# Kernel tuning notes

Hardware: AMD Instinct MI355X
Metric: run time of the kernel (lower is better)

Reference implementation:

```python
import jax, jax.numpy as jnp
import numpy as np

B, S, H, I, E = 4, 4096, 1024, 4096, 4
VOCAB = 32000


def setup_inputs() -> dict:
    key = jax.random.key(0)
    k1, k2, k3, k4, k5 = jax.random.split(key, 5)
    scale = 1.0 / np.sqrt(H)
    return {
        "hidden_states": jax.random.normal(k1, (B, S, H), dtype=jnp.float32),
        "gate_proj": jax.random.normal(k2, (E, H, I), dtype=jnp.float32) * scale,
        "up_proj": jax.random.normal(k3, (E, H, I), dtype=jnp.float32) * scale,
        "down_proj": jax.random.normal(k4, (E, I, H), dtype=jnp.float32) * (1.0 / np.sqrt(I)),
        "token_ids": jax.random.randint(k5, (B, S), 0, VOCAB, dtype=jnp.int64),
    }


def reference(hidden_states, gate_proj, up_proj, down_proj, token_ids):
    # hidden_states: [B, S, H]; token_ids: [B, S]
    num_experts = gate_proj.shape[0]
    expert_ids = token_ids % num_experts  # [B, S]
    out = jnp.zeros_like(hidden_states)
    for e in range(num_experts):  # small fixed expert loop
        gate = jax.nn.silu(jnp.einsum("bsh,hi->bsi", hidden_states, gate_proj[e]))
        up = jnp.einsum("bsh,hi->bsi", hidden_states, up_proj[e])
        y = jnp.einsum("bsi,ih->bsh", gate * up, down_proj[e])
        out = jnp.where((expert_ids == e)[..., None], y, out)
    return out
```

## Files before the change

### kernel.cpp

```cpp
#include <hip/hip_runtime.h>

#define TOK    16384
#define HD     1024
#define ID     4096
#define NE     4
#define MAXMT  131
#define MAXMT2 67
#define NKT    (HD / 64)

typedef __attribute__((ext_vector_type(4))) float f32x4;
typedef __attribute__((ext_vector_type(8))) short bf16x8;
typedef unsigned int u32;

static __device__ __forceinline__ unsigned short f2bf(float f) {
  unsigned u = __float_as_uint(f);
  u += 0x7FFFu + ((u >> 16) & 1u);
  return (unsigned short)(u >> 16);
}

static __device__ __forceinline__ void gl16(const void* g, void* l) {
  __builtin_amdgcn_global_load_lds((const __attribute__((address_space(1))) u32*)g,
                                   (__attribute__((address_space(3))) u32*)l, 16, 0, 0);
}

static __device__ __forceinline__ void barx() {
  asm volatile("" ::: "memory");
  __builtin_amdgcn_s_barrier();
  asm volatile("" ::: "memory");
}

__global__ void k_route0(const int* __restrict__ ids, int* __restrict__ meta) {
  __shared__ int cnt[4];
  int t = threadIdx.x;
  if (t < 4) cnt[t] = 0;
  __syncthreads();
  int l0 = 0, l1 = 0, l2 = 0, l3 = 0;
  for (int i = t; i < TOK; i += 256) {
    int e = ids[i] & 3;
    l0 += (e == 0); l1 += (e == 1); l2 += (e == 2); l3 += (e == 3);
  }
  atomicAdd(&cnt[0], l0); atomicAdd(&cnt[1], l1);
  atomicAdd(&cnt[2], l2); atomicAdd(&cnt[3], l3);
  __syncthreads();
  if (t == 0) {
    int o = 0;
    for (int e = 0; e < 4; ++e) { meta[e] = o; meta[8 + e] = o; o += cnt[e]; }
    meta[4] = o;
  }
}

__global__ void k_route1(const int* __restrict__ ids, int* __restrict__ meta,
                         int* __restrict__ perm) {
  int i = blockIdx.x * 256 + threadIdx.x;
  if (i < TOK) {
    int e = ids[i] & 3;
    int s = atomicAdd(&meta[8 + e], 1);
    perm[s] = i;
  }
}

__global__ void k_pre(const float* __restrict__ gw, const float* __restrict__ uw,
                      const float* __restrict__ dw, const float* __restrict__ hs,
                      unsigned short* __restrict__ gT, unsigned short* __restrict__ uT,
                      unsigned short* __restrict__ dT, unsigned short* __restrict__ hid) {
  int z = blockIdx.y;
  int t = threadIdx.x;
  if (z >= 12) {
    int i = ((z - 12) * 1024 + blockIdx.x) * 256 + t;
    const f32x4* p = (const f32x4*)(hs + ((size_t)i << 3));
    f32x4 a = p[0], b = p[1];
    union { unsigned short u[8]; uint4 q; } o;
    o.u[0] = f2bf(a.x); o.u[1] = f2bf(a.y); o.u[2] = f2bf(a.z); o.u[3] = f2bf(a.w);
    o.u[4] = f2bf(b.x); o.u[5] = f2bf(b.y); o.u[6] = f2bf(b.z); o.u[7] = f2bf(b.w);
    *(uint4*)(hid + ((size_t)i << 3)) = o.q;
    return;
  }
  __shared__ float tile[64][65];
  const float* s; unsigned short* d; int R, C, lg;
  if (z < 8) {
    R = HD; C = ID; lg = 6;
    int m = z & 3;
    if (z < 4) { s = gw + (size_t)m * R * C; d = gT + (size_t)m * R * C; }
    else       { s = uw + (size_t)m * R * C; d = uT + (size_t)m * R * C; }
  } else {
    R = ID; C = HD; lg = 4;
    int m = z - 8;
    s = dw + (size_t)m * R * C; d = dT + (size_t)m * R * C;
  }
  int bx = blockIdx.x;
  int tx = bx & ((1 << lg) - 1), ty = bx >> lg;
  int r0 = ty << 6, c0 = tx << 6;
  int lr = t >> 4, lc = (t & 15) << 2;
  #pragma unroll
  for (int it = 0; it < 4; ++it) {
    int r = lr + (it << 4);
    f32x4 v = *(const f32x4*)(s + (size_t)(r0 + r) * C + c0 + lc);
    tile[r][lc] = v.x; tile[r][lc + 1] = v.y; tile[r][lc + 2] = v.z; tile[r][lc + 3] = v.w;
  }
  __syncthreads();
  int c = t >> 2, rb = (t & 3) << 4;
  union { unsigned short u[16]; uint4 q[2]; } o;
  #pragma unroll
  for (int j = 0; j < 16; ++j) o.u[j] = f2bf(tile[rb + j][c]);
  uint4* dp = (uint4*)(d + (size_t)(c0 + c) * R + r0 + rb);
  dp[0] = o.q[0]; dp[1] = o.q[1];
}

#define MFMA16 __builtin_amdgcn_mfma_f32_16x16x32_bf16

#define RD_A(MH, KX, D) { _Pragma("unroll") for (int m = 0; m < 4; ++m) \
  fa[m] = *(const bf16x8*)(smem + (D) + ((offA[m] + (MH) * 8192) ^ ((KX) << 6))); }
#define RD_B(KX, D) { _Pragma("unroll") for (int n = 0; n < 4; ++n) \
  fb[n] = *(const bf16x8*)(smem + (D) + (offB[n] ^ ((KX) << 6))); }
#define STG_A(HH, TILE, D) { _Pragma("unroll") for (int j = (HH) * 2; j < (HH) * 2 + 2; ++j) \
  gl16(srcA[j] + (TILE) * 64, smem + (D) + dstA[j]); }
#define STG_B(HH, TILE, D) { _Pragma("unroll") for (int j = (HH) * 2; j < (HH) * 2 + 2; ++j) \
  gl16(srcB[j] + (TILE) * 64, smem + (D) + dstB[j]); }
#define PH_TAIL(MH) barx(); \
  asm volatile("s_waitcnt lgkmcnt(0)" ::: "memory"); \
  __builtin_amdgcn_sched_barrier(0); \
  __builtin_amdgcn_s_setprio(1); \
  { _Pragma("unroll") for (int m = 0; m < 4; ++m) \
    _Pragma("unroll") for (int n = 0; n < 4; ++n) \
      acc[(MH) * 4 + m][n] = MFMA16(fa[m], fb[n], acc[(MH) * 4 + m][n], 0, 0, 0); } \
  __builtin_amdgcn_s_setprio(0)

__global__ __launch_bounds__(512, 2) void k_gemm1(
    const unsigned short* __restrict__ hid,
    const unsigned short* __restrict__ gT,
    const unsigned short* __restrict__ uT,
    const int* __restrict__ meta,
    const int* __restrict__ perm,
    unsigned short* __restrict__ act) {
  extern __shared__ __align__(16) char smem[];
  int offs[5];
  #pragma unroll
  for (int i = 0; i < 5; ++i) offs[i] = meta[i];
  int bid = blockIdx.x;
  int logical = (bid & 7) * (MAXMT2 * 32 / 8) + (bid >> 3);
  int mt = logical >> 5;
  int ny = logical & 31;
  int e = -1, mloc = 0, base = 0;
  #pragma unroll
  for (int ee = 0; ee < 4; ++ee) {
    int tiles = (offs[ee + 1] - offs[ee] + 255) >> 8;
    if (e < 0 && mt < base + tiles) { e = ee; mloc = mt - base; }
    base += tiles;
  }
  if (e < 0) return;
  int slot0 = offs[e] + (mloc << 8);
  int send = offs[e + 1];
  int tid = threadIdx.x, lane = tid & 63, wid = tid >> 6;
  int n0 = ny << 7;

  int rsub = lane >> 3;
  int ke = ((lane & 7) ^ rsub) << 3;
  const unsigned short* srcA[4];
  const unsigned short* srcB[4];
  int dstA[4], dstB[4];
  const unsigned short* gb = gT + (size_t)e * ID * HD;
  const unsigned short* ub = uT + (size_t)e * ID * HD;
  #pragma unroll
  for (int j = 0; j < 4; ++j) {
    int r = j * 64 + wid * 8 + rsub;
    int slot = slot0 + r;
    int pr = perm[slot < send ? slot : slot0];
    srcA[j] = hid + (size_t)pr * HD + ke;
    dstA[j] = j * 8192 + wid * 1024;
    int rb = r;
    int s = rb >> 4;
    int grow = n0 + ((s >> 1) << 4) + (rb & 15);
    srcB[j] = ((s & 1) ? ub : gb) + (size_t)grow * HD + ke;
    dstB[j] = 32768 + j * 8192 + wid * 1024;
  }

  int wm = wid >> 2, wn = wid & 3;
  int r16 = lane & 15, kg = lane >> 4;
  int offA[4], offB[4];
  #pragma unroll
  for (int m = 0; m < 4; ++m) {
    int row = wm * 128 + m * 16 + r16;
    offA[m] = row * 128 + ((kg << 4) ^ ((row & 7) << 4));
  }
  #pragma unroll
  for (int n = 0; n < 4; ++n) {
    int row = wn * 64 + n * 16 + r16;
    offB[n] = 32768 + row * 128 + ((kg << 4) ^ ((row & 7) << 4));
  }

  f32x4 acc[8][4];
  #pragma unroll
  for (int m = 0; m < 8; ++m)
    #pragma unroll
    for (int n = 0; n < 4; ++n) acc[m][n] = (f32x4){0.f, 0.f, 0.f, 0.f};
  bf16x8 fa[4], fb[4];

  STG_B(0, 0, 0);
  STG_A(0, 0, 0); STG_A(1, 0, 0);
  STG_B(1, 0, 0);
  STG_B(0, 1, 65536);
  asm volatile("s_waitcnt vmcnt(2)" ::: "memory");
  barx();

  #pragma unroll 1
  for (int i = 0; i < NKT / 2 - 1; ++i) {
    int t1 = 2 * i + 1, t2 = 2 * i + 2, t3 = 2 * i + 3;
    RD_A(0, 0, 0); RD_B(0, 0);
    STG_B(1, t1, 65536);
    PH_TAIL(0); barx();
    RD_A(1, 0, 0);
    STG_A(0, t1, 65536); STG_A(1, t1, 65536);
    PH_TAIL(1); barx();
    RD_A(0, 1, 0); RD_B(1, 0);
    PH_TAIL(0); barx();
    RD_A(1, 1, 0);
    STG_B(0, t2, 0);
    PH_TAIL(1);
    asm volatile("s_waitcnt vmcnt(2)" ::: "memory");
    barx();
    RD_A(0, 0, 65536); RD_B(0, 65536);
    STG_A(0, t2, 0); STG_A(1, t2, 0);
    PH_TAIL(0); barx();
    RD_A(1, 0, 65536);
    STG_B(1, t2, 0);
    PH_TAIL(1); barx();
    RD_A(0, 1, 65536); RD_B(1, 65536);
    PH_TAIL(0); barx();
    RD_A(1, 1, 65536);
    STG_B(0, t3, 65536);
    PH_TAIL(1);
    asm volatile("s_waitcnt vmcnt(2)" ::: "memory");
    barx();
  }
  {
    RD_A(0, 0, 0); RD_B(0, 0);
    STG_B(1, 15, 65536);
    PH_TAIL(0); barx();
    RD_A(1, 0, 0);
    STG_A(0, 15, 65536); STG_A(1, 15, 65536);
    PH_TAIL(1); barx();
    RD_A(0, 1, 0); RD_B(1, 0);
    PH_TAIL(0); barx();
    RD_A(1, 1, 0);
    PH_TAIL(1);
    asm volatile("s_waitcnt vmcnt(0)" ::: "memory");
    barx();
    RD_A(0, 0, 65536); RD_B(0, 65536);
    PH_TAIL(0); barx();
    RD_A(1, 0, 65536);
    PH_TAIL(1); barx();
    RD_A(0, 1, 65536); RD_B(1, 65536);
    PH_TAIL(0); barx();
    RD_A(1, 1, 65536);
    PH_TAIL(1);
  }

  #pragma unroll
  for (int mf = 0; mf < 8; ++mf) {
    int lr = wm * 128 + mf * 16 + kg * 4;
    #pragma unroll
    for (int np = 0; np < 2; ++np) {
      int col = n0 + (2 * wn + np) * 16 + r16;
      #pragma unroll
      for (int r = 0; r < 4; ++r) {
        int slot = slot0 + lr + r;
        if (slot < send) {
          float g = acc[mf][2 * np][r];
          float u = acc[mf][2 * np + 1][r];
          float y = (g / (1.f + __expf(-g))) * u;
          act[(size_t)slot * ID + col] = f2bf(y);
        }
      }
    }
  }
}

__global__ __launch_bounds__(256, 2) void k_gemm2(
    const unsigned short* __restrict__ act,
    const unsigned short* __restrict__ dT,
    const int* __restrict__ meta,
    const int* __restrict__ perm,
    float* __restrict__ out) {
  __shared__ unsigned short As[128 * 64];
  __shared__ unsigned short Bs[128 * 64];
  int offs[5];
  #pragma unroll
  for (int i = 0; i < 5; ++i) offs[i] = meta[i];
  int bid = blockIdx.x;
  int logical = (bid & 7) * (MAXMT * 8 / 8) + (bid >> 3);
  int mt = logical >> 3;
  int nyy = logical & 7;
  int e = -1, mloc = 0, base = 0;
  #pragma unroll
  for (int ee = 0; ee < 4; ++ee) {
    int tiles = (offs[ee + 1] - offs[ee] + 127) >> 7;
    if (e < 0 && mt < base + tiles) { e = ee; mloc = mt - base; }
    base += tiles;
  }
  if (e < 0) return;
  int slot0 = offs[e] + (mloc << 7);
  int send = offs[e + 1];
  int tid = threadIdx.x;
  int n0 = nyy << 7;
  const unsigned short* dbase = dT + (size_t)e * HD * ID;
  const unsigned short* ap[4];
  const unsigned short* bp[4];
  int wofs[4];
  #pragma unroll
  for (int it = 0; it < 4; ++it) {
    int b = (tid << 4) + (it << 12);
    int row = b >> 7;
    int kob = b & 127;
    int slot = slot0 + row;
    int s2 = slot < send ? slot : slot0;
    ap[it] = act + (size_t)s2 * ID + (kob >> 1);
    bp[it] = dbase + (size_t)(n0 + row) * ID + (kob >> 1);
    wofs[it] = row * 64 + ((kob ^ ((row & 7) << 4)) >> 1);
  }
  int lane = tid & 63, wid = tid >> 6;
  int wm = wid >> 1, wn = wid & 1;
  int r16 = lane & 15, kg = lane >> 4;
  f32x4 zero = {0.f, 0.f, 0.f, 0.f};
  f32x4 acc[4][4];
  #pragma unroll
  for (int m = 0; m < 4; ++m)
    #pragma unroll
    for (int n = 0; n < 4; ++n) acc[m][n] = zero;

  bf16x8 sa[4], sb[4];
  #pragma unroll
  for (int it = 0; it < 4; ++it) {
    sa[it] = *(const bf16x8*)(ap[it]);
    sb[it] = *(const bf16x8*)(bp[it]);
  }
  for (int kt = 0; kt < ID / 64; ++kt) {
    __syncthreads();
    #pragma unroll
    for (int it = 0; it < 4; ++it) {
      *(bf16x8*)(As + wofs[it]) = sa[it];
      *(bf16x8*)(Bs + wofs[it]) = sb[it];
    }
    __syncthreads();
    if (kt < ID / 64 - 1) {
      int ko = (kt + 1) << 6;
      #pragma unroll
      for (int it = 0; it < 4; ++it) {
        sa[it] = *(const bf16x8*)(ap[it] + ko);
        sb[it] = *(const bf16x8*)(bp[it] + ko);
      }
    }
    #pragma unroll
    for (int kk = 0; kk < 2; ++kk) {
      bf16x8 fa[4], fb[4];
      #pragma unroll
      for (int m = 0; m < 4; ++m) {
        int row = (wm << 6) + (m << 4) + r16;
        int kob = (kk << 6) + (kg << 4);
        fa[m] = *(const bf16x8*)(As + row * 64 + ((kob ^ ((row & 7) << 4)) >> 1));
      }
      #pragma unroll
      for (int n = 0; n < 4; ++n) {
        int row = (wn << 6) + (n << 4) + r16;
        int kob = (kk << 6) + (kg << 4);
        fb[n] = *(const bf16x8*)(Bs + row * 64 + ((kob ^ ((row & 7) << 4)) >> 1));
      }
      #pragma unroll
      for (int m = 0; m < 4; ++m)
        #pragma unroll
        for (int n = 0; n < 4; ++n)
          acc[m][n] = __builtin_amdgcn_mfma_f32_16x16x32_bf16(fa[m], fb[n], acc[m][n], 0, 0, 0);
    }
  }
  #pragma unroll
  for (int m = 0; m < 4; ++m) {
    int lr = (wm << 6) + (m << 4) + (kg << 2);
    int pr4[4];
    #pragma unroll
    for (int r = 0; r < 4; ++r) {
      int slot = slot0 + lr + r;
      pr4[r] = slot < send ? perm[slot] : -1;
    }
    #pragma unroll
    for (int n = 0; n < 4; ++n) {
      int col = n0 + (wn << 6) + (n << 4) + r16;
      #pragma unroll
      for (int r = 0; r < 4; ++r) {
        if (pr4[r] >= 0) out[(size_t)pr4[r] * HD + col] = acc[m][n][r];
      }
    }
  }
}

extern "C" void kernel_launch(void* const* d_in, const int* in_sizes, int n_in,
                              void* d_out, int out_size, void* d_ws, size_t ws_size,
                              hipStream_t stream) {
  const float* hs = (const float*)d_in[0];
  const float* gw = (const float*)d_in[1];
  const float* uw = (const float*)d_in[2];
  const float* dw = (const float*)d_in[3];
  const int* ids = (const int*)d_in[4];
  float* out = (float*)d_out;

  char* w = (char*)d_ws;
  size_t o = 0;
  int* meta = (int*)(w + o); o += 64;
  int* perm = (int*)(w + o); o += (size_t)TOK * 4;
  o = (o + 255) & ~(size_t)255;
  unsigned short* hid = (unsigned short*)(w + o); o += (size_t)TOK * HD * 2;
  unsigned short* gT  = (unsigned short*)(w + o); o += (size_t)NE * ID * HD * 2;
  unsigned short* uT  = (unsigned short*)(w + o); o += (size_t)NE * ID * HD * 2;
  unsigned short* dT  = (unsigned short*)(w + o); o += (size_t)NE * ID * HD * 2;
  unsigned short* actb = (unsigned short*)(w + o); o += (size_t)TOK * ID * 2;

  hipFuncSetAttribute((const void*)k_gemm1,
                      hipFuncAttributeMaxDynamicSharedMemorySize, 131072);

  hipLaunchKernelGGL(k_route0, dim3(1), dim3(256), 0, stream, ids, meta);
  hipLaunchKernelGGL(k_route1, dim3(TOK / 256), dim3(256), 0, stream, ids, meta, perm);
  hipLaunchKernelGGL(k_pre, dim3(1024, 20), dim3(256), 0, stream,
                     gw, uw, dw, hs, gT, uT, dT, hid);
  hipLaunchKernelGGL(k_gemm1, dim3(MAXMT2 * 32), dim3(512), 131072, stream,
                     hid, gT, uT, meta, perm, actb);
  hipLaunchKernelGGL(k_gemm2, dim3(MAXMT * 8), dim3(256), 0, stream,
                     actb, dT, meta, perm, out);
}
```

Baseline: 644.3 us.

## Convert both expert GEMMs to persistent kernels with atomic tile queues

Both GEMM kernels now launch a fixed grid (256 and 512 workgroups) and loop, pulling tile indices from a global atomic counter that the routing kernel resets each call. The goal is to cut the cost of launching many empty or padded workgroups and to balance load across CUs dynamically. The old XCD-aware bid swizzle is gone, so tiles are handed out in linear order. That may hurt L2 locality on the multi-XCD chip, and each tile now pays for an extra atomic and two barriers.

Result: slower. 692.3 us (+7.4%).

```diff
diff --git a/kernel.cpp b/kernel.cpp
--- a/kernel.cpp
+++ b/kernel.cpp
@@ -7,6 +7,8 @@
 #define MAXMT  131
 #define MAXMT2 67
 #define NKT    (HD / 64)
+#define NT1    (MAXMT2 * 32)
+#define NT2    (MAXMT * 8)
 
 typedef __attribute__((ext_vector_type(4))) float f32x4;
 typedef __attribute__((ext_vector_type(8))) short bf16x8;
@@ -29,7 +31,8 @@
   asm volatile("" ::: "memory");
 }
 
-__global__ void k_route0(const int* __restrict__ ids, int* __restrict__ meta) {
+__global__ void k_route0(const int* __restrict__ ids, int* __restrict__ meta,
+                         int* __restrict__ ctrs) {
   __shared__ int cnt[4];
   int t = threadIdx.x;
   if (t < 4) cnt[t] = 0;
@@ -46,6 +49,8 @@
     int o = 0;
     for (int e = 0; e < 4; ++e) { meta[e] = o; meta[8 + e] = o; o += cnt[e]; }
     meta[4] = o;
+    ctrs[0] = 0;
+    ctrs[1] = 0;
   }
 }
 
@@ -131,49 +136,23 @@
     const unsigned short* __restrict__ uT,
     const int* __restrict__ meta,
     const int* __restrict__ perm,
-    unsigned short* __restrict__ act) {
+    unsigned short* __restrict__ act,
+    int* ctr) {
   extern __shared__ __align__(16) char smem[];
+  __shared__ int s_t;
   int offs[5];
   #pragma unroll
   for (int i = 0; i < 5; ++i) offs[i] = meta[i];
-  int bid = blockIdx.x;
-  int logical = (bid & 7) * (MAXMT2 * 32 / 8) + (bid >> 3);
-  int mt = logical >> 5;
-  int ny = logical & 31;
-  int e = -1, mloc = 0, base = 0;
-  #pragma unroll
-  for (int ee = 0; ee < 4; ++ee) {
-    int tiles = (offs[ee + 1] - offs[ee] + 255) >> 8;
-    if (e < 0 && mt < base + tiles) { e = ee; mloc = mt - base; }
-    base += tiles;
-  }
-  if (e < 0) return;
-  int slot0 = offs[e] + (mloc << 8);
-  int send = offs[e + 1];
   int tid = threadIdx.x, lane = tid & 63, wid = tid >> 6;
-  int n0 = ny << 7;
 
   int rsub = lane >> 3;
   int ke = ((lane & 7) ^ rsub) << 3;
-  const unsigned short* srcA[4];
-  const unsigned short* srcB[4];
   int dstA[4], dstB[4];
-  const unsigned short* gb = gT + (size_t)e * ID * HD;
-  const unsigned short* ub = uT + (size_t)e * ID * HD;
   #pragma unroll
   for (int j = 0; j < 4; ++j) {
-    int r = j * 64 + wid * 8 + rsub;
-    int slot = slot0 + r;
-    int pr = perm[slot < send ? slot : slot0];
-    srcA[j] = hid + (size_t)pr * HD + ke;
     dstA[j] = j * 8192 + wid * 1024;
-    int rb = r;
-    int s = rb >> 4;
-    int grow = n0 + ((s >> 1) << 4) + (rb & 15);
-    srcB[j] = ((s & 1) ? ub : gb) + (size_t)grow * HD + ke;
     dstB[j] = 32768 + j * 8192 + wid * 1024;
   }
-
   int wm = wid >> 2, wn = wid & 3;
   int r16 = lane & 15, kg = lane >> 4;
   int offA[4], offB[4];
@@ -187,88 +166,124 @@
     int row = wn * 64 + n * 16 + r16;
     offB[n] = 32768 + row * 128 + ((kg << 4) ^ ((row & 7) << 4));
   }
-
-  f32x4 acc[8][4];
-  #pragma unroll
-  for (int m = 0; m < 8; ++m)
-    #pragma unroll
-    for (int n = 0; n < 4; ++n) acc[m][n] = (f32x4){0.f, 0.f, 0.f, 0.f};
   bf16x8 fa[4], fb[4];
 
-  STG_B(0, 0, 0);
-  STG_A(0, 0, 0); STG_A(1, 0, 0);
-  STG_B(1, 0, 0);
-  STG_B(0, 1, 65536);
-  asm volatile("s_waitcnt vmcnt(2)" ::: "memory");
-  barx();
-
-  #pragma unroll 1
-  for (int i = 0; i < NKT / 2 - 1; ++i) {
-    int t1 = 2 * i + 1, t2 = 2 * i + 2, t3 = 2 * i + 3;
-    RD_A(0, 0, 0); RD_B(0, 0);
-    STG_B(1, t1, 65536);
-    PH_TAIL(0); barx();
-    RD_A(1, 0, 0);
-    STG_A(0, t1, 65536); STG_A(1, t1, 65536);
-    PH_TAIL(1); barx();
-    RD_A(0, 1, 0); RD_B(1, 0);
-    PH_TAIL(0); barx();
-    RD_A(1, 1, 0);
-    STG_B(0, t2, 0);
-    PH_TAIL(1);
+  for (;;) {
+    __syncthreads();
+    if (tid == 0) s_t = atomicAdd(ctr, 1);
+    __syncthreads();
+    int tt = s_t;
+    if (tt >= NT1) break;
+    int mt = tt >> 5;
+    int ny = tt & 31;
+    int e = -1, mloc = 0, base = 0;
+    #pragma unroll
+    for (int ee = 0; ee < 4; ++ee) {
+      int tiles = (offs[ee + 1] - offs[ee] + 255) >> 8;
+      if (e < 0 && mt < base + tiles) { e = ee; mloc = mt - base; }
+      base += tiles;
+    }
+    if (e < 0) continue;
+    int slot0 = offs[e] + (mloc << 8);
+    int send = offs[e + 1];
+    int n0 = ny << 7;
+
+    const unsigned short* srcA[4];
+    const unsigned short* srcB[4];
+    const unsigned short* gb = gT + (size_t)e * ID * HD;
+    const unsigned short* ub = uT + (size_t)e * ID * HD;
+    #pragma unroll
+    for (int j = 0; j < 4; ++j) {
+      int r = j * 64 + wid * 8 + rsub;
+      int slot = slot0 + r;
+      int pr = perm[slot < send ? slot : slot0];
+      srcA[j] = hid + (size_t)pr * HD + ke;
+      int s = r >> 4;
+      int grow = n0 + ((s >> 1) << 4) + (r & 15);
+      srcB[j] = ((s & 1) ? ub : gb) + (size_t)grow * HD + ke;
+    }
+
+    f32x4 acc[8][4];
+    #pragma unroll
+    for (int m = 0; m < 8; ++m)
+      #pragma unroll
+      for (int n = 0; n < 4; ++n) acc[m][n] = (f32x4){0.f, 0.f, 0.f, 0.f};
+
+    STG_B(0, 0, 0);
+    STG_A(0, 0, 0); STG_A(1, 0, 0);
+    STG_B(1, 0, 0);
+    STG_B(0, 1, 65536);
     asm volatile("s_waitcnt vmcnt(2)" ::: "memory");
     barx();
-    RD_A(0, 0, 65536); RD_B(0, 65536);
-    STG_A(0, t2, 0); STG_A(1, t2, 0);
-    PH_TAIL(0); barx();
-    RD_A(1, 0, 65536);
-    STG_B(1, t2, 0);
-    PH_TAIL(1); barx();
-    RD_A(0, 1, 65536); RD_B(1, 65536);
-    PH_TAIL(0); barx();
-    RD_A(1, 1, 65536);
-    STG_B(0, t3, 65536);
-    PH_TAIL(1);
-    asm volatile("s_waitcnt vmcnt(2)" ::: "memory");
-    barx();
-  }
-  {
-    RD_A(0, 0, 0); RD_B(0, 0);
-    STG_B(1, 15, 65536);
-    PH_TAIL(0); barx();
-    RD_A(1, 0, 0);
-    STG_A(0, 15, 65536); STG_A(1, 15, 65536);
-    PH_TAIL(1); barx();
-    RD_A(0, 1, 0); RD_B(1, 0);
-    PH_TAIL(0); barx();
-    RD_A(1, 1, 0);
-    PH_TAIL(1);
-    asm volatile("s_waitcnt vmcnt(0)" ::: "memory");
-    barx();
-    RD_A(0, 0, 65536); RD_B(0, 65536);
-    PH_TAIL(0); barx();
-    RD_A(1, 0, 65536);
-    PH_TAIL(1); barx();
-    RD_A(0, 1, 65536); RD_B(1, 65536);
-    PH_TAIL(0); barx();
-    RD_A(1, 1, 65536);
-    PH_TAIL(1);
-  }
-
-  #pragma unroll
-  for (int mf = 0; mf < 8; ++mf) {
-    int lr = wm * 128 + mf * 16 + kg * 4;
-    #pragma unroll
-    for (int np = 0; np < 2; ++np) {
-      int col = n0 + (2 * wn + np) * 16 + r16;
-      #pragma unroll
-      for (int r = 0; r < 4; ++r) {
-        int slot = slot0 + lr + r;
-        if (slot < send) {
-          float g = acc[mf][2 * np][r];
-          float u = acc[mf][2 * np + 1][r];
-          float y = (g / (1.f + __expf(-g))) * u;
-          act[(size_t)slot * ID + col] = f2bf(y);
+
+    #pragma unroll 1
+    for (int i = 0; i < NKT / 2 - 1; ++i) {
+      int t1 = 2 * i + 1, t2 = 2 * i + 2, t3 = 2 * i + 3;
+      RD_A(0, 0, 0); RD_B(0, 0);
+      STG_B(1, t1, 65536);
+      PH_TAIL(0); barx();
+      RD_A(1, 0, 0);
+      STG_A(0, t1, 65536); STG_A(1, t1, 65536);
+      PH_TAIL(1); barx();
+      RD_A(0, 1, 0); RD_B(1, 0);
+      PH_TAIL(0); barx();
+      RD_A(1, 1, 0);
+      STG_B(0, t2, 0);
+      PH_TAIL(1);
+      asm volatile("s_waitcnt vmcnt(2)" ::: "memory");
+      barx();
+      RD_A(0, 0, 65536); RD_B(0, 65536);
+      STG_A(0, t2, 0); STG_A(1, t2, 0);
+      PH_TAIL(0); barx();
+      RD_A(1, 0, 65536);
+      STG_B(1, t2, 0);
+      PH_TAIL(1); barx();
+      RD_A(0, 1, 65536); RD_B(1, 65536);
+      PH_TAIL(0); barx();
+      RD_A(1, 1, 65536);
+      STG_B(0, t3, 65536);
+      PH_TAIL(1);
+      asm volatile("s_waitcnt vmcnt(2)" ::: "memory");
+      barx();
+    }
+    {
+      RD_A(0, 0, 0); RD_B(0, 0);
+      STG_B(1, 15, 65536);
+      PH_TAIL(0); barx();
+      RD_A(1, 0, 0);
+      STG_A(0, 15, 65536); STG_A(1, 15, 65536);
+      PH_TAIL(1); barx();
+      RD_A(0, 1, 0); RD_B(1, 0);
+      PH_TAIL(0); barx();
+      RD_A(1, 1, 0);
+      PH_TAIL(1);
+      asm volatile("s_waitcnt vmcnt(0)" ::: "memory");
+      barx();
+      RD_A(0, 0, 65536); RD_B(0, 65536);
+      PH_TAIL(0); barx();
+      RD_A(1, 0, 65536);
+      PH_TAIL(1); barx();
+      RD_A(0, 1, 65536); RD_B(1, 65536);
+      PH_TAIL(0); barx();
+      RD_A(1, 1, 65536);
+      PH_TAIL(1);
+    }
+
+    #pragma unroll
+    for (int mf = 0; mf < 8; ++mf) {
+      int lr = wm * 128 + mf * 16 + kg * 4;
+      #pragma unroll
+      for (int np = 0; np < 2; ++np) {
+        int col = n0 + (2 * wn + np) * 16 + r16;
+        #pragma unroll
+        for (int r = 0; r < 4; ++r) {
+          int slot = slot0 + lr + r;
+          if (slot < send) {
+            float g = acc[mf][2 * np][r];
+            float u = acc[mf][2 * np + 1][r];
+            float y = (g / (1.f + __expf(-g))) * u;
+            act[(size_t)slot * ID + col] = f2bf(y);
+          }
         }
       }
     }
@@ -280,112 +295,125 @@
     const unsigned short* __restrict__ dT,
     const int* __restrict__ meta,
     const int* __restrict__ perm,
-    float* __restrict__ out) {
+    float* __restrict__ out,
+    int* ctr) {
   __shared__ unsigned short As[128 * 64];
   __shared__ unsigned short Bs[128 * 64];
+  __shared__ int s_t;
   int offs[5];
   #pragma unroll
   for (int i = 0; i < 5; ++i) offs[i] = meta[i];
-  int bid = blockIdx.x;
-  int logical = (bid & 7) * (MAXMT * 8 / 8) + (bid >> 3);
-  int mt = logical >> 3;
-  int nyy = logical & 7;
-  int e = -1, mloc = 0, base = 0;
-  #pragma unroll
-  for (int ee = 0; ee < 4; ++ee) {
-    int tiles = (offs[ee + 1] - offs[ee] + 127) >> 7;
-    if (e < 0 && mt < base + tiles) { e = ee; mloc = mt - base; }
-    base += tiles;
-  }
-  if (e < 0) return;
-  int slot0 = offs[e] + (mloc << 7);
-  int send = offs[e + 1];
   int tid = threadIdx.x;
-  int n0 = nyy << 7;
-  const unsigned short* dbase = dT + (size_t)e * HD * ID;
-  const unsigned short* ap[4];
-  const unsigned short* bp[4];
+  int lane = tid & 63, wid = tid >> 6;
+  int wm = wid >> 1, wn = wid & 1;
+  int r16 = lane & 15, kg = lane >> 4;
   int wofs[4];
   #pragma unroll
   for (int it = 0; it < 4; ++it) {
     int b = (tid << 4) + (it << 12);
     int row = b >> 7;
     int kob = b & 127;
-    int slot = slot0 + row;
-    int s2 = slot < send ? slot : slot0;
-    ap[it] = act + (size_t)s2 * ID + (kob >> 1);
-    bp[it] = dbase + (size_t)(n0 + row) * ID + (kob >> 1);
     wofs[it] = row * 64 + ((kob ^ ((row & 7) << 4)) >> 1);
   }
-  int lane = tid & 63, wid = tid >> 6;
-  int wm = wid >> 1, wn = wid & 1;
-  int r16 = lane & 15, kg = lane >> 4;
-  f32x4 zero = {0.f, 0.f, 0.f, 0.f};
-  f32x4 acc[4][4];
-  #pragma unroll
-  for (int m = 0; m < 4; ++m)
-    #pragma unroll
-    for (int n = 0; n < 4; ++n) acc[m][n] = zero;
-
-  bf16x8 sa[4], sb[4];
-  #pragma unroll
-  for (int it = 0; it < 4; ++it) {
-    sa[it] = *(const bf16x8*)(ap[it]);
-    sb[it] = *(const bf16x8*)(bp[it]);
-  }
-  for (int kt = 0; kt < ID / 64; ++kt) {
+
+  for (;;) {
     __syncthreads();
+    if (tid == 0) s_t = atomicAdd(ctr, 1);
+    __syncthreads();
+    int tt = s_t;
+    if (tt >= NT2) break;
+    int mt = tt >> 3;
+    int nyy = tt & 7;
+    int e = -1, mloc = 0, base = 0;
+    #pragma unroll
+    for (int ee = 0; ee < 4; ++ee) {
+      int tiles = (offs[ee + 1] - offs[ee] + 127) >> 7;
+      if (e < 0 && mt < base + tiles) { e = ee; mloc = mt - base; }
+      base += tiles;
+    }
+    if (e < 0) continue;
+    int slot0 = offs[e] + (mloc << 7);
+    int send = offs[e + 1];
+    int n0 = nyy << 7;
+    const unsigned short* dbase = dT + (size_t)e * HD * ID;
+    const unsigned short* ap[4];
+    const unsigned short* bp[4];
     #pragma unroll
     for (int it = 0; it < 4; ++it) {
-      *(bf16x8*)(As + wofs[it]) = sa[it];
-      *(bf16x8*)(Bs + wofs[it]) = sb[it];
-    }
-    __syncthreads();
-    if (kt < ID / 64 - 1) {
-      int ko = (kt + 1) << 6;
+      int b = (tid << 4) + (it << 12);
+      int row = b >> 7;
+      int kob = b & 127;
+      int slot = slot0 + row;
+      int s2 = slot < send ? slot : slot0;
+      ap[it] = act + (size_t)s2 * ID + (kob >> 1);
+      bp[it] = dbase + (size_t)(n0 + row) * ID + (kob >> 1);
+    }
+    f32x4 acc[4][4];
+    #pragma unroll
+    for (int m = 0; m < 4; ++m)
+      #pragma unroll
+      for (int n = 0; n < 4; ++n) acc[m][n] = (f32x4){0.f, 0.f, 0.f, 0.f};
+
+    bf16x8 sa[4], sb[4];
+    #pragma unroll
+    for (int it = 0; it < 4; ++it) {
+      sa[it] = *(const bf16x8*)(ap[it]);
+      sb[it] = *(const bf16x8*)(bp[it]);
+    }
+    for (int kt = 0; kt < ID / 64; ++kt) {
+      __syncthreads();
       #pragma unroll
       for (int it = 0; it < 4; ++it) {
-        sa[it] = *(const bf16x8*)(ap[it] + ko);
-        sb[it] = *(const bf16x8*)(bp[it] + ko);
-      }
-    }
-    #pragma unroll
-    for (int kk = 0; kk < 2; ++kk) {
-      bf16x8 fa[4], fb[4];
-      #pragma unroll
-      for (int m = 0; m < 4; ++m) {
-        int row = (wm << 6) + (m << 4) + r16;
-        int kob = (kk << 6) + (kg << 4);
-        fa[m] = *(const bf16x8*)(As + row * 64 + ((kob ^ ((row & 7) << 4)) >> 1));
+        *(bf16x8*)(As + wofs[it]) = sa[it];
+        *(bf16x8*)(Bs + wofs[it]) = sb[it];
+      }
+      __syncthreads();
+      if (kt < ID / 64 - 1) {
+        int ko = (kt + 1) << 6;
+        #pragma unroll
+        for (int it = 0; it < 4; ++it) {
+          sa[it] = *(const bf16x8*)(ap[it] + ko);
+          sb[it] = *(const bf16x8*)(bp[it] + ko);
+        }
+      }
+      #pragma unroll
+      for (int kk = 0; kk < 2; ++kk) {
+        bf16x8 fa[4], fb[4];
+        #pragma unroll
+        for (int m = 0; m < 4; ++m) {
+          int row = (wm << 6) + (m << 4) + r16;
+          int kob = (kk << 6) + (kg << 4);
+          fa[m] = *(const bf16x8*)(As + row * 64 + ((kob ^ ((row & 7) << 4)) >> 1));
+        }
+        #pragma unroll
+        for (int n = 0; n < 4; ++n) {
+          int row = (wn << 6) + (n << 4) + r16;
+          int kob = (kk << 6) + (kg << 4);
+          fb[n] = *(const bf16x8*)(Bs + row * 64 + ((kob ^ ((row & 7) << 4)) >> 1));
+        }
+        #pragma unroll
+        for (int m = 0; m < 4; ++m)
+          #pragma unroll
+          for (int n = 0; n < 4; ++n)
+            acc[m][n] = __builtin_amdgcn_mfma_f32_16x16x32_bf16(fa[m], fb[n], acc[m][n], 0, 0, 0);
+      }
+    }
+    #pragma unroll
+    for (int m = 0; m < 4; ++m) {
+      int lr = (wm << 6) + (m << 4) + (kg << 2);
+      int pr4[4];
+      #pragma unroll
+      for (int r = 0; r < 4; ++r) {
+        int slot = slot0 + lr + r;
+        pr4[r] = slot < send ? perm[slot] : -1;
       }
       #pragma unroll
       for (int n = 0; n < 4; ++n) {
-        int row = (wn << 6) + (n << 4) + r16;
-        int kob = (kk << 6) + (kg << 4);
-        fb[n] = *(const bf16x8*)(Bs + row * 64 + ((kob ^ ((row & 7) << 4)) >> 1));
-      }
-      #pragma unroll
-      for (int m = 0; m < 4; ++m)
-        #pragma unroll
-        for (int n = 0; n < 4; ++n)
-          acc[m][n] = __builtin_amdgcn_mfma_f32_16x16x32_bf16(fa[m], fb[n], acc[m][n], 0, 0, 0);
-    }
-  }
-  #pragma unroll
-  for (int m = 0; m < 4; ++m) {
-    int lr = (wm << 6) + (m << 4) + (kg << 2);
-    int pr4[4];
-    #pragma unroll
-    for (int r = 0; r < 4; ++r) {
-      int slot = slot0 + lr + r;
-      pr4[r] = slot < send ? perm[slot] : -1;
-    }
-    #pragma unroll
-    for (int n = 0; n < 4; ++n) {
-      int col = n0 + (wn << 6) + (n << 4) + r16;
-      #pragma unroll
-      for (int r = 0; r < 4; ++r) {
-        if (pr4[r] >= 0) out[(size_t)pr4[r] * HD + col] = acc[m][n][r];
+        int col = n0 + (wn << 6) + (n << 4) + r16;
+        #pragma unroll
+        for (int r = 0; r < 4; ++r) {
+          if (pr4[r] >= 0) out[(size_t)pr4[r] * HD + col] = acc[m][n][r];
+        }
       }
     }
   }
@@ -404,6 +432,7 @@
   char* w = (char*)d_ws;
   size_t o = 0;
   int* meta = (int*)(w + o); o += 64;
+  int* ctrs = (int*)(w + o); o += 64;
   int* perm = (int*)(w + o); o += (size_t)TOK * 4;
   o = (o + 255) & ~(size_t)255;
   unsigned short* hid = (unsigned short*)(w + o); o += (size_t)TOK * HD * 2;
@@ -415,12 +444,12 @@
   hipFuncSetAttribute((const void*)k_gemm1,
                       hipFuncAttributeMaxDynamicSharedMemorySize, 131072);
 
-  hipLaunchKernelGGL(k_route0, dim3(1), dim3(256), 0, stream, ids, meta);
+  hipLaunchKernelGGL(k_route0, dim3(1), dim3(256), 0, stream, ids, meta, ctrs);
   hipLaunchKernelGGL(k_route1, dim3(TOK / 256), dim3(256), 0, stream, ids, meta, perm);
   hipLaunchKernelGGL(k_pre, dim3(1024, 20), dim3(256), 0, stream,
                      gw, uw, dw, hs, gT, uT, dT, hid);
-  hipLaunchKernelGGL(k_gemm1, dim3(MAXMT2 * 32), dim3(512), 131072, stream,
-                     hid, gT, uT, meta, perm, actb);
-  hipLaunchKernelGGL(k_gemm2, dim3(MAXMT * 8), dim3(256), 0, stream,
-                     actb, dT, meta, perm, out);
-}
+  hipLaunchKernelGGL(k_gemm1, dim3(256), dim3(512), 131072, stream,
+                     hid, gT, uT, meta, perm, actb, &ctrs[0]);
+  hipLaunchKernelGGL(k_gemm2, dim3(512), dim3(256), 0, stream,
+                     actb, dT, meta, perm, out, &ctrs[1]);
+}
```
